# Kernel tuning notes

Measured on AMD Instinct MI355X. Metric: run time of the kernel, lower is better.

Reference implementation:

```python
import jax, jax.numpy as jnp
import numpy as np

PATCH = 16


def setup_inputs() -> dict:
    key = jax.random.key(0)
    x = jax.random.normal(key, (256, 3, 224, 224), dtype=jnp.float32)
    return {"x": x}


def reference(x):
    P = PATCH
    B, C, Hi, Wi = x.shape
    h, w = Hi // P, Wi // P  # grid rows (h) and cols (w)
    # 'b c (h p1) (w p2) -> b w h p1 p2 c'
    patches = x.reshape(B, C, h, P, w, P).transpose(0, 4, 2, 3, 5, 1)  # (B, w, h, p1, p2, C)
    # center_rotate: transpose p1<->p2 for patches with grid col j in [w/3, 2w/3]
    # and grid row k in [h/3, 2h/3] (original skips j < W/3 or j > 2W/3, same for k)
    jw = jnp.arange(w)
    kh = jnp.arange(h)
    mw = (jw >= w / 3) & (jw <= 2 * w / 3)
    mh = (kh >= h / 3) & (kh <= 2 * h / 3)
    mask = (mw[:, None] & mh[None, :])[None, :, :, None, None, None]  # (1, w, h, 1, 1, 1)
    rot = jnp.where(mask, jnp.swapaxes(patches, 3, 4), patches)  # (B, w, h, a3, a4, C)
    # 'b w h p2 p1 c -> b c (h p2) (w p1)': axis3 is read as p2 (inner height),
    # axis4 as p1 (inner width) -- i.e. every patch gets transposed on reassembly,
    # so center patches (transposed twice) come back in original orientation.
    out = rot.transpose(0, 5, 2, 3, 1, 4).reshape(B, C, h * P, w * P)
    return out
```

## Files before the change

### kernel.cpp

```cpp
#include <hip/hip_runtime.h>


#define HH 224
#define WW 224
#define W4 56

typedef float vf4 __attribute__((ext_vector_type(4)));

__global__ __launch_bounds__(256) void patch_rotate_kernel(
    const float* __restrict__ x, float* __restrict__ out, int n4) {
  int idx = blockIdx.x * blockDim.x + threadIdx.x;
  if (idx >= n4) return;

  int bc   = idx / (HH * W4);
  int rem  = idx % (HH * W4);
  int row  = rem / W4;
  int col4 = rem % W4;

  int k = row >> 4;
  int j = col4 >> 2;

  bool center = (j >= 5) & (j <= 9) & (k >= 5) & (k <= 9);

  if (!center) {
    vf4 v = __builtin_nontemporal_load((const vf4*)x + idx);
    __builtin_nontemporal_store(v, (vf4*)out + idx);
  } else {
    int a3  = row & 15;
    int a4b = (col4 & 3) << 2;
    int base = (bc * HH + (k << 4)) * WW + (j << 4) + a3;
    vf4 v;
    v.x = x[base + (a4b + 0) * WW];
    v.y = x[base + (a4b + 1) * WW];
    v.z = x[base + (a4b + 2) * WW];
    v.w = x[base + (a4b + 3) * WW];
    *((vf4*)out + idx) = v;
  }
}

extern "C" void kernel_launch(void* const* d_in, const int* in_sizes, int n_in,
                              void* d_out, int out_size, void* d_ws, size_t ws_size,
                              hipStream_t stream) {
  const float* x = (const float*)d_in[0];
  float* out = (float*)d_out;
  int n4 = out_size / 4;
  int threads = 256;
  int blocks = (n4 + threads - 1) / threads;
  patch_rotate_kernel<<<blocks, threads, 0, stream>>>(x, out, n4);
}
```

Before: 257.2 us.

## Split identity copy and center-patch transpose into separate LDS-staged block roles

Partitions the grid so most blocks do a plain nontemporal vector copy of non-center elements, and extra blocks each transpose four center patches through shared memory. The center path now uses coalesced vectorized loads and stores instead of strided scalar gathers. The cost is an extra launch region, a barrier, and LDS traffic. Shapes are hardcoded to this input size.

```diff
diff --git a/kernel.cpp b/kernel.cpp
--- a/kernel.cpp
+++ b/kernel.cpp
@@ -1,41 +1,62 @@
 #include <hip/hip_runtime.h>
 
 
-#define HH 224
-#define WW 224
 #define W4 56
+#define IMG_F4 12544
+#define NIDENT_BLKS 37632
 
 typedef float vf4 __attribute__((ext_vector_type(4)));
 
 __global__ __launch_bounds__(256) void patch_rotate_kernel(
-    const float* __restrict__ x, float* __restrict__ out, int n4) {
-  int idx = blockIdx.x * blockDim.x + threadIdx.x;
-  if (idx >= n4) return;
+    const float* __restrict__ x, float* __restrict__ out) {
+  const int tid = threadIdx.x;
 
-  int bc   = idx / (HH * W4);
-  int rem  = idx % (HH * W4);
-  int row  = rem / W4;
-  int col4 = rem % W4;
+  if (blockIdx.x < NIDENT_BLKS) {
+    const int idx = blockIdx.x * 256 + tid;
+    const int rem = idx % IMG_F4;
+    const int row = rem / W4;
+    const int col4 = rem % W4;
+    const int k = row >> 4;
+    const int j = col4 >> 2;
+    const bool center = (j >= 5) & (j <= 9) & (k >= 5) & (k <= 9);
+    if (!center) {
+      vf4 v = __builtin_nontemporal_load((const vf4*)x + idx);
+      __builtin_nontemporal_store(v, (vf4*)out + idx);
+    }
+    return;
+  }
 
-  int k = row >> 4;
-  int j = col4 >> 2;
+  __shared__ float ldsT[4][16][20];
+  const int pb = blockIdx.x - NIDENT_BLKS;
+  const int lp = tid >> 6;
+  const int l  = tid & 63;
+  const int p  = pb * 4 + lp;
+  const int q  = p / 25;
+  const int pi = p % 25;
+  const int kk = 5 + pi / 5;
+  const int jj = 5 + pi % 5;
+  const float* __restrict__ xs = x + (size_t)q * (IMG_F4 * 4);
+  float* __restrict__ os = out + (size_t)q * (IMG_F4 * 4);
 
-  bool center = (j >= 5) & (j <= 9) & (k >= 5) & (k <= 9);
+  const int r  = l >> 2;
+  const int c0 = (l & 3) << 2;
 
-  if (!center) {
-    vf4 v = __builtin_nontemporal_load((const vf4*)x + idx);
-    __builtin_nontemporal_store(v, (vf4*)out + idx);
-  } else {
-    int a3  = row & 15;
-    int a4b = (col4 & 3) << 2;
-    int base = (bc * HH + (k << 4)) * WW + (j << 4) + a3;
-    vf4 v;
-    v.x = x[base + (a4b + 0) * WW];
-    v.y = x[base + (a4b + 1) * WW];
-    v.z = x[base + (a4b + 2) * WW];
-    v.w = x[base + (a4b + 3) * WW];
-    *((vf4*)out + idx) = v;
-  }
+  const vf4 v = __builtin_nontemporal_load(
+      (const vf4*)(xs + (kk * 16 + r) * 224 + jj * 16 + c0));
+  ldsT[lp][c0 + 0][r] = v.x;
+  ldsT[lp][c0 + 1][r] = v.y;
+  ldsT[lp][c0 + 2][r] = v.z;
+  ldsT[lp][c0 + 3][r] = v.w;
+
+  __syncthreads();
+
+  vf4 w;
+  w.x = ldsT[lp][r][c0 + 0];
+  w.y = ldsT[lp][r][c0 + 1];
+  w.z = ldsT[lp][r][c0 + 2];
+  w.w = ldsT[lp][r][c0 + 3];
+  __builtin_nontemporal_store(
+      w, (vf4*)(os + (kk * 16 + r) * 224 + jj * 16 + c0));
 }
 
 extern "C" void kernel_launch(void* const* d_in, const int* in_sizes, int n_in,
@@ -43,8 +64,6 @@
                               hipStream_t stream) {
   const float* x = (const float*)d_in[0];
   float* out = (float*)d_out;
-  int n4 = out_size / 4;
-  int threads = 256;
-  int blocks = (n4 + threads - 1) / threads;
-  patch_rotate_kernel<<<blocks, threads, 0, stream>>>(x, out, n4);
+  const int blocks = NIDENT_BLKS + 4800;
+  patch_rotate_kernel<<<blocks, 256, 0, stream>>>(x, out);
 }
```

New measurement: 251.8 us. 1.02x faster.
